# Kernel optimization log

Hardware: AMD Instinct MI355X
Metric: run time of the kernel (lower is better)

Reference implementation:

```python
import jax, jax.numpy as jnp
import numpy as np

B, N, D, H = 2, 384, 128, 8

def _ln(x, g, b, eps=1e-5):
    m = jnp.mean(x, -1, keepdims=True)
    v = jnp.mean((x - m) ** 2, -1, keepdims=True)
    return (x - m) * jax.lax.rsqrt(v + eps) * g + b

def _gelu(x):
    return jax.nn.gelu(x, approximate=False)  # torch nn.GELU default = exact erf

def setup_inputs() -> dict:
    key = jax.random.key(0)
    ks = jax.random.split(key, 20)
    def w(i, *s):
        return jax.random.normal(ks[i], s, jnp.float32) * 0.02
    return {
        'node_features': jax.random.normal(ks[0], (B, N, D), jnp.float32),
        'edge_features': jax.random.normal(ks[1], (B, N, N, D), jnp.float32),
        'mask': jnp.ones((B, N), dtype=bool),
        'attn_wqkv_node': w(2, D, 3 * D),
        'attn_wqkv_edge': w(3, D, 4 * D),
        'lin0_w': w(4, D, D), 'lin0_b': jnp.zeros(D, jnp.float32),
        'ln0_g': jnp.ones(D, jnp.float32), 'ln0_bias': jnp.zeros(D, jnp.float32),
        'ln1_g': jnp.ones(D, jnp.float32), 'ln1_bias': jnp.zeros(D, jnp.float32),
        'nmlp_w1': w(5, D, 2 * D), 'nmlp_w2': w(6, 2 * D, D), 'nmlp_b2': jnp.zeros(D, jnp.float32),
        'e0_we': w(7, 2 * D, D), 'e0_be': jnp.zeros(D, jnp.float32),
        'e0_ws': w(8, D, D), 'e0_bs': jnp.zeros(D, jnp.float32),
        'e0_wt': w(9, D, D), 'e0_bt': jnp.zeros(D, jnp.float32),
        'e0_wer': w(10, D, D), 'e0_wec': w(11, D, D),
        'e0_w1': w(12, D, D), 'e0_b1': jnp.zeros(D, jnp.float32),
        'e1_w1': w(13, D, 2 * D), 'e1_w2': w(14, 2 * D, D), 'e1_b2': jnp.zeros(D, jnp.float32),
        'eln0_g': jnp.ones(D, jnp.float32), 'eln0_b': jnp.zeros(D, jnp.float32),
        'eln1_g': jnp.ones(D, jnp.float32), 'eln1_b': jnp.zeros(D, jnp.float32),
    }

def _forward(node, edge, wqkv_n, wqkv_e, lin0_w, lin0_b, ln0_g, ln0_bias, ln1_g, ln1_bias,
             nmlp_w1, nmlp_w2, nmlp_b2, e0_we, e0_be, e0_ws, e0_bs, e0_wt, e0_bt,
             e0_wer, e0_wec, e0_w1, e0_b1, e1_w1, e1_w2, e1_b2, eln0_g, eln0_b, eln1_g, eln1_b):
    b, n, d = node.shape
    h = H
    dh = d // h
    scale = 1.0 / (d ** 0.5)  # note: scale uses full d_hid as in source
    # ---- RTAttention (modulate_v=True) ----
    qkv_n = (node @ wqkv_n).reshape(b, n, h, 3 * dh).transpose(0, 2, 1, 3)  # b h n 3dh
    qn, kn, vn = jnp.split(qkv_n, 3, axis=-1)
    qkv_e = (edge @ wqkv_e).reshape(b, n, n, h, 4 * dh).transpose(0, 3, 1, 2, 4)  # b h i j 4dh
    eq, ek, ev, em = jnp.split(qkv_e, 4, axis=-1)
    q = qn[:, :, :, None, :] + eq                      # b h i j dh
    k = kn[:, :, None, :, :] + ek
    v = vn[:, :, None, :, :] * em + ev                 # modulate_v: v_node*edge[3] + edge[2]
    dots = scale * jnp.einsum('bhijd,bhijd->bhij', q, k)
    attn = jax.nn.softmax(dots, axis=-1)
    out = jnp.einsum('bhij,bhijd->bhid', attn, v)
    out = out.transpose(0, 2, 1, 3).reshape(b, n, d)
    # ---- node updates, type 'rt' (dropout=0 -> identity) ----
    x = _ln(node + (out @ lin0_w + lin0_b), ln0_g, ln0_bias)
    x = _ln(x + (_gelu(x @ nmlp_w1) @ nmlp_w2 + nmlp_b2), ln1_g, ln1_bias)
    # ---- edge updates: EdgeMLP ----
    sn = (x @ e0_ws + e0_bs)[:, :, None, :]                       # broadcast over j
    tn = (x @ e0_wt + e0_bt)[:, None, :, :]                       # broadcast over i
    se = jnp.mean(edge, axis=1, keepdims=True) @ e0_wec           # mean over dim -3, lin0_ec
    te = jnp.mean(edge, axis=2, keepdims=True) @ e0_wer           # mean over dim -2, lin0_er
    e = jnp.concatenate([edge, jnp.swapaxes(edge, 1, 2)], axis=-1) @ e0_we + e0_be
    e = _gelu(e + sn + tn + se + te) @ e0_w1 + e0_b1
    edge2 = _ln(edge + e, eln0_g, eln0_b)
    edge2 = _ln(edge2 + (_gelu(edge2 @ e1_w1) @ e1_w2 + e1_b2), eln1_g, eln1_b)
    return x, edge2

def reference(node_features, edge_features, mask, attn_wqkv_node, attn_wqkv_edge,
              lin0_w, lin0_b, ln0_g, ln0_bias, ln1_g, ln1_bias,
              nmlp_w1, nmlp_w2, nmlp_b2, e0_we, e0_be, e0_ws, e0_bs, e0_wt, e0_bt,
              e0_wer, e0_wec, e0_w1, e0_b1, e1_w1, e1_w2, e1_b2,
              eln0_g, eln0_b, eln1_g, eln1_b):
    # mask is accepted but unused by the source forward path
    return _forward(node_features, edge_features, attn_wqkv_node, attn_wqkv_edge,
                    lin0_w, lin0_b, ln0_g, ln0_bias, ln1_g, ln1_bias,
                    nmlp_w1, nmlp_w2, nmlp_b2, e0_we, e0_be, e0_ws, e0_bs, e0_wt, e0_bt,
                    e0_wer, e0_wec, e0_w1, e0_b1, e1_w1, e1_w2, e1_b2,
                    eln0_g, eln0_b, eln1_g, eln1_b)
```

## Files before the change

### kernel.cpp

```cpp
#include <hip/hip_runtime.h>
#include <hip/hip_bf16.h>
#include <cstdint>
#include <cstddef>

#define B_ 2
#define N_ 384
#define D_ 128
#define NN (N_*N_)
#define BN (B_*N_)
#define EDGE_ELEMS (B_*NN*D_)
#define NODE_ELEMS (BN*D_)

typedef short bh8 __attribute__((ext_vector_type(8)));
typedef float f32x4 __attribute__((ext_vector_type(4)));

__device__ __forceinline__ f32x4 mfma_bf16(bh8 a, bh8 b, f32x4 c){
  return __builtin_amdgcn_mfma_f32_16x16x32_bf16(a, b, c, 0, 0, 0);
}
__device__ __forceinline__ unsigned short f2bf(float f){
  unsigned u = __float_as_uint(f);
  return (unsigned short)((u + 0x7fffu + ((u >> 16) & 1u)) >> 16);
}
__device__ __forceinline__ unsigned f2bf_pk(float a, float b){
  __hip_bfloat162 h = __float22bfloat162_rn(make_float2(a, b));
  return *(unsigned*)&h;
}
__device__ __forceinline__ float bf2f(unsigned short h){
  return __uint_as_float(((unsigned)h) << 16);
}
__device__ __forceinline__ float geluf(float x){
  return 0.5f * x * (1.0f + erff(x * 0.70710678118654752f));
}
__device__ __forceinline__ float gelu_fast(float x){
  float x2 = x * x;
  float t  = __fmaf_rn(0.044715f * x, x2, x);
  float e  = __expf(1.5957691216057308f * t);
  float r  = __builtin_amdgcn_rcpf(e + 1.0f);
  return x - x * r;
}
__device__ __forceinline__ f32x4 zero4(){ f32x4 z = {0.f,0.f,0.f,0.f}; return z; }

__global__ void kprep(const float* wqkv_e, const float* e0_we, const float* e0_w1,
                      const float* e1_w1, const float* e1_w2,
                      const float* node, const float* wqkv_n,
                      unsigned short* WqkvT, unsigned short* WeT, unsigned short* W1T,
                      unsigned short* E1W1T, unsigned short* E1W2T,
                      float* qkvn){
  int m = blockIdx.y;
  int tid = threadIdx.x;
  if (m < 5){
    const float* src; unsigned short* dst; int K, Nn;
    if (m == 0){ src = wqkv_e; dst = WqkvT; K = 128; Nn = 512; }
    else if (m == 1){ src = e0_we; dst = WeT;   K = 256; Nn = 128; }
    else if (m == 2){ src = e0_w1; dst = W1T;   K = 128; Nn = 128; }
    else if (m == 3){ src = e1_w1; dst = E1W1T; K = 128; Nn = 256; }
    else            { src = e1_w2; dst = E1W2T; K = 256; Nn = 128; }
    int idx = blockIdx.x * 384 + tid;
    if (idx < K * Nn){
      int n = idx / K, k = idx % K;
      dst[idx] = f2bf(src[k * Nn + n]);
    }
  } else {
    int row = blockIdx.x;
    __shared__ float sn[128];
    if (tid < 128) sn[tid] = node[row * 128 + tid];
    __syncthreads();
    float acc = 0.f;
    #pragma unroll 8
    for (int k = 0; k < 128; ++k) acc += sn[k] * wqkv_n[k * 384 + tid];
    qkvn[row * 384 + tid] = acc;
  }
}

__global__ void kprepA(const float* __restrict__ edge, unsigned short* __restrict__ E16,
                       float* __restrict__ meanJ){
  __shared__ float red[8][128];
  int bi = blockIdx.x; int tid = threadIdx.x;
  const float4* src = (const float4*)(edge + (size_t)bi * N_ * D_);
  uint2* gdst = (uint2*)E16 + (size_t)bi * (N_ * D_ / 4);
  float ps0 = 0.f, ps1 = 0.f, ps2 = 0.f, ps3 = 0.f;
  #pragma unroll 4
  for (int k = 0; k < 48; ++k){
    int idx = k * 256 + tid;
    float4 v = src[idx];
    uint2 o;
    o.x = f2bf_pk(v.x, v.y);
    o.y = f2bf_pk(v.z, v.w);
    gdst[idx] = o;
    ps0 += v.x; ps1 += v.y; ps2 += v.z; ps3 += v.w;
  }
  int g = tid >> 5, d0 = (tid & 31) * 4;
  red[g][d0] = ps0; red[g][d0 + 1] = ps1; red[g][d0 + 2] = ps2; red[g][d0 + 3] = ps3;
  __syncthreads();
  if (tid < 128){
    float s = 0.f;
    #pragma unroll
    for (int gg = 0; gg < 8; ++gg) s += red[gg][tid];
    meanJ[bi * 128 + tid] = s * (1.0f / N_);
  }
}

__global__ __launch_bounds__(256, 2) void kattnI(
    const unsigned short* __restrict__ E16, const unsigned short* __restrict__ WqkvT,
    const float* __restrict__ qkvn, float* __restrict__ attn,
    float* __restrict__ meanI){
  __shared__ float red[16][128];
  int tid = threadIdx.x;
  if (blockIdx.y == 1){
    int bj = blockIdx.x; int b = bj / N_, j = bj % N_;
    int ig = tid >> 4, dsub = tid & 15;
    float acc[8];
    #pragma unroll
    for (int e = 0; e < 8; ++e) acc[e] = 0.f;
    #pragma unroll 4
    for (int i = ig; i < N_; i += 16){
      const unsigned short* p = E16 + ((size_t)(b * N_ + i) * N_ + j) * D_ + dsub * 8;
      uint4 u = *(const uint4*)p;
      acc[0] += bf2f((unsigned short)(u.x & 0xffff)); acc[1] += bf2f((unsigned short)(u.x >> 16));
      acc[2] += bf2f((unsigned short)(u.y & 0xffff)); acc[3] += bf2f((unsigned short)(u.y >> 16));
      acc[4] += bf2f((unsigned short)(u.z & 0xffff)); acc[5] += bf2f((unsigned short)(u.z >> 16));
      acc[6] += bf2f((unsigned short)(u.w & 0xffff)); acc[7] += bf2f((unsigned short)(u.w >> 16));
    }
    #pragma unroll
    for (int e = 0; e < 8; ++e) red[ig][dsub * 8 + e] = acc[e];
    __syncthreads();
    if (tid < 128){
      float s = 0.f;
      #pragma unroll
      for (int gg = 0; gg < 16; ++gg) s += red[gg][tid];
      meanI[bj * 128 + tid] = s * (1.0f / N_);
    }
    return;
  }
  int bi = blockIdx.x; int b = bi / N_;
  int w = tid >> 6, lane = tid & 63, quad = lane >> 4, c16 = lane & 15;
  const float scale = 0.08838834764831845f;
  const unsigned short* Abase = E16 + (size_t)bi * N_ * D_;

  bh8 bf[2][4][4];
  #pragma unroll
  for (int s = 0; s < 2; ++s){
    int h = w + s * 4;
    #pragma unroll
    for (int u = 0; u < 4; ++u)
      #pragma unroll
      for (int ks = 0; ks < 4; ++ks){
        int col = h * 64 + u * 16 + c16;
        bf[s][u][ks] = *(const bh8*)(WqkvT + col * 128 + ks * 32 + quad * 8);
      }
  }
  float qv[2];
  #pragma unroll
  for (int s = 0; s < 2; ++s) qv[s] = qkvn[bi * 384 + (w + s * 4) * 48 + c16];

  float m_run[2] = {-1e30f, -1e30f}, l_run[2] = {0.f, 0.f}, o[2] = {0.f, 0.f};
  bh8 af[4];
  #pragma unroll
  for (int ks = 0; ks < 4; ++ks)
    af[ks] = *(const bh8*)(Abase + (size_t)c16 * D_ + ks * 32 + quad * 8);

  for (int jt = 0; jt < 24; ++jt){
    int jn = (jt + 1 < 24) ? jt + 1 : 0;
    bh8 afn[4];
    #pragma unroll
    for (int ks = 0; ks < 4; ++ks)
      afn[ks] = *(const bh8*)(Abase + (size_t)(jn * 16 + c16) * D_ + ks * 32 + quad * 8);
    float knv[2][4], vnv[2][4];
    const float* kvb = qkvn + ((size_t)b * N_ + jt * 16 + quad * 4) * 384;
    #pragma unroll
    for (int s = 0; s < 2; ++s)
      #pragma unroll
      for (int r = 0; r < 4; ++r){
        knv[s][r] = kvb[r * 384 + (w + s * 4) * 48 + 16 + c16];
        vnv[s][r] = kvb[r * 384 + (w + s * 4) * 48 + 32 + c16];
      }
    f32x4 EQ[2], EK[2], EV[2], EM[2];
    #pragma unroll
    for (int s = 0; s < 2; ++s){ EQ[s] = zero4(); EK[s] = zero4(); EV[s] = zero4(); EM[s] = zero4(); }
    #pragma unroll
    for (int ks = 0; ks < 4; ++ks)
      #pragma unroll
      for (int s = 0; s < 2; ++s){
        EQ[s] = mfma_bf16(af[ks], bf[s][0][ks], EQ[s]);
        EK[s] = mfma_bf16(af[ks], bf[s][1][ks], EK[s]);
        EV[s] = mfma_bf16(af[ks], bf[s][2][ks], EV[s]);
        EM[s] = mfma_bf16(af[ks], bf[s][3][ks], EM[s]);
      }
    #pragma unroll
    for (int s = 0; s < 2; ++s){
      float dots[4], vv[4];
      #pragma unroll
      for (int r = 0; r < 4; ++r){
        float t1 = (qv[s] + EQ[s][r]) * (knv[s][r] + EK[s][r]);
        t1 += __shfl_xor(t1, 1); t1 += __shfl_xor(t1, 2);
        t1 += __shfl_xor(t1, 4); t1 += __shfl_xor(t1, 8);
        dots[r] = t1 * scale;
        vv[r] = vnv[s][r] * EM[s][r] + EV[s][r];
      }
      float tmax = fmaxf(fmaxf(dots[0], dots[1]), fmaxf(dots[2], dots[3]));
      tmax = fmaxf(tmax, __shfl_xor(tmax, 16));
      tmax = fmaxf(tmax, __shfl_xor(tmax, 32));
      float mnew = fmaxf(m_run[s], tmax);
      float al = __expf(m_run[s] - mnew);
      float p0 = __expf(dots[0] - mnew), p1 = __expf(dots[1] - mnew);
      float p2 = __expf(dots[2] - mnew), p3 = __expf(dots[3] - mnew);
      float lt = p0 + p1 + p2 + p3;
      lt += __shfl_xor(lt, 16); lt += __shfl_xor(lt, 32);
      l_run[s] = l_run[s] * al + lt;
      m_run[s] = mnew;
      o[s] = o[s] * al + p0 * vv[0] + p1 * vv[1] + p2 * vv[2] + p3 * vv[3];
    }
    #pragma unroll
    for (int ks = 0; ks < 4; ++ks) af[ks] = afn[ks];
  }
  #pragma unroll
  for (int s = 0; s < 2; ++s){
    float oo = o[s];
    oo += __shfl_xor(oo, 16); oo += __shfl_xor(oo, 32);
    oo /= l_run[s];
    if (quad == 0) attn[(size_t)bi * D_ + (w + s * 4) * 16 + c16] = oo;
  }
}

__global__ void knodeadd(const float* __restrict__ node, const float* __restrict__ attn,
                         const float* lin0_w, const float* lin0_b,
                         const float* g0, const float* bb0,
                         const float* w1, const float* w2, const float* b2,
                         const float* g1, const float* bb1,
                         const float* __restrict__ meanJ, const float* __restrict__ meanI,
                         const float* ws, const float* bs, const float* wt, const float* bt,
                         const float* wer, const float* wec, const float* be,
                         float* __restrict__ xOut,
                         float* __restrict__ rowAdd, float* __restrict__ colAdd){
  int row = blockIdx.x; int tid = threadIdx.x;
  __shared__ float sa[128], sx[128], sh[256], rb[8], sx2[128], smJ[128], smI[128];
  if (tid < 128){
    sa[tid] = attn[row * 128 + tid];
    smJ[tid] = meanJ[row * 128 + tid];
    smI[tid] = meanI[row * 128 + tid];
  }
  __syncthreads();
  float y = 0.f, x0 = 0.f;
  if (tid < 128){
    float acc = lin0_b[tid];
    #pragma unroll 8
    for (int k = 0; k < 128; ++k) acc += sa[k] * lin0_w[k * 128 + tid];
    y = acc + node[row * 128 + tid];
  }
  { float sv = (tid < 128) ? y : 0.f, sq = (tid < 128) ? y * y : 0.f;
    #pragma unroll
    for (int m2 = 32; m2 >= 1; m2 >>= 1){ sv += __shfl_xor(sv, m2); sq += __shfl_xor(sq, m2); }
    if ((tid & 63) == 0){ rb[tid >> 6] = sv; rb[4 + (tid >> 6)] = sq; } }
  __syncthreads();
  float mean = (rb[0] + rb[1] + rb[2] + rb[3]) * (1.f / 128.f);
  float var  = (rb[4] + rb[5] + rb[6] + rb[7]) * (1.f / 128.f) - mean * mean;
  float rstd = rsqrtf(var + 1e-5f);
  if (tid < 128){ x0 = (y - mean) * rstd * g0[tid] + bb0[tid]; sx[tid] = x0; }
  __syncthreads();
  { float acc = 0.f;
    #pragma unroll 8
    for (int k = 0; k < 128; ++k) acc += sx[k] * w1[k * 256 + tid];
    sh[tid] = geluf(acc); }
  __syncthreads();
  float y2 = 0.f;
  if (tid < 128){
    float acc = b2[tid];
    #pragma unroll 8
    for (int e = 0; e < 256; ++e) acc += sh[e] * w2[e * 128 + tid];
    y2 = acc + x0;
  }
  __syncthreads();
  { float sv = (tid < 128) ? y2 : 0.f, sq = (tid < 128) ? y2 * y2 : 0.f;
    #pragma unroll
    for (int m2 = 32; m2 >= 1; m2 >>= 1){ sv += __shfl_xor(sv, m2); sq += __shfl_xor(sq, m2); }
    if ((tid & 63) == 0){ rb[tid >> 6] = sv; rb[4 + (tid >> 6)] = sq; } }
  __syncthreads();
  mean = (rb[0] + rb[1] + rb[2] + rb[3]) * (1.f / 128.f);
  var  = (rb[4] + rb[5] + rb[6] + rb[7]) * (1.f / 128.f) - mean * mean;
  rstd = rsqrtf(var + 1e-5f);
  if (tid < 128){
    float xv = (y2 - mean) * rstd * g1[tid] + bb1[tid];
    xOut[row * 128 + tid] = xv;
    sx2[tid] = xv;
  }
  __syncthreads();
  if (tid < 128){
    int d = tid;
    float s1 = bs[d], s3 = 0.f;
    #pragma unroll 8
    for (int k = 0; k < 128; ++k){
      s1 += sx2[k] * ws[k * 128 + d];
      s3 += smJ[k] * wer[k * 128 + d];
    }
    rowAdd[row * 128 + d] = s1 + s3 + be[d];
  } else {
    int d = tid - 128;
    float s2 = bt[d], s4 = 0.f;
    #pragma unroll 8
    for (int k = 0; k < 128; ++k){
      s2 += sx2[k] * wt[k * 128 + d];
      s4 += smI[k] * wec[k * 128 + d];
    }
    colAdd[row * 128 + d] = s2 + s4;
  }
}

__global__ __launch_bounds__(256, 3) void kedge4(
    const unsigned short* __restrict__ E16, const unsigned short* __restrict__ WeT,
    const unsigned short* __restrict__ W1T, const unsigned short* __restrict__ E1W1T,
    const unsigned short* __restrict__ E1W2T,
    const float* __restrict__ rowAdd, const float* __restrict__ colAdd,
    const float* __restrict__ b1, const float* __restrict__ eg0, const float* __restrict__ eb0,
    const float* __restrict__ e1b2, const float* __restrict__ eg1, const float* __restrict__ eb1,
    float* __restrict__ eOut){
  __shared__ unsigned short sA[64][264];
  __shared__ unsigned short sT[64][136];
  __shared__ float lrS[4][64], lrQ[4][64];
  int tid = threadIdx.x;
  int w = tid >> 6, lane = tid & 63, quad = lane >> 4, c16 = lane & 15;
  int R0 = blockIdx.x * 64;
  int b = R0 / NN; int rem = R0 % NN; int i = rem / N_; int j0 = rem % N_;

  bh8 wb1[2][8];
  #pragma unroll
  for (int t = 0; t < 2; ++t)
    #pragma unroll
    for (int ks = 0; ks < 8; ++ks){
      int col = w * 32 + t * 16 + c16;
      wb1[t][ks] = *(const bh8*)(WeT + (size_t)col * 256 + ks * 32 + quad * 8);
    }
  float ca[2][16], rAv[2];
  #pragma unroll
  for (int t = 0; t < 2; ++t){
    rAv[t] = rowAdd[(b * N_ + i) * D_ + w * 32 + t * 16 + c16];
    #pragma unroll
    for (int ms = 0; ms < 4; ++ms)
      #pragma unroll
      for (int r = 0; r < 4; ++r)
        ca[t][ms * 4 + r] = colAdd[(size_t)(b * N_ + j0 + ms * 16 + quad * 4 + r) * D_
                                   + w * 32 + t * 16 + c16];
  }

  #pragma unroll
  for (int it = 0; it < 8; ++it){
    int cid = it * 256 + tid;
    int rrow = cid >> 5;
    int kc = (cid & 31) * 8;
    const unsigned short* sp;
    if (kc < 128) sp = E16 + ((size_t)(b * N_ + i) * N_ + (j0 + rrow)) * D_ + kc;
    else          sp = E16 + ((size_t)(b * N_ + j0 + rrow) * N_ + i) * D_ + (kc - 128);
    *(float4*)&sA[rrow][kc] = *(const float4*)sp;
  }
  __syncthreads();

  f32x4 acc1[2][4];
  #pragma unroll
  for (int t = 0; t < 2; ++t) for (int ms = 0; ms < 4; ++ms) acc1[t][ms] = zero4();
  #pragma unroll
  for (int ks = 0; ks < 8; ++ks){
    bh8 af[4];
    #pragma unroll
    for (int ms = 0; ms < 4; ++ms)
      af[ms] = *(const bh8*)&sA[ms * 16 + c16][ks * 32 + quad * 8];
    #pragma unroll
    for (int t = 0; t < 2; ++t)
      #pragma unroll
      for (int ms = 0; ms < 4; ++ms)
        acc1[t][ms] = mfma_bf16(af[ms], wb1[t][ks], acc1[t][ms]);
  }
  #pragma unroll
  for (int ms = 0; ms < 4; ++ms)
    #pragma unroll
    for (int r = 0; r < 4; ++r){
      int m = ms * 16 + quad * 4 + r;
      float v0 = gelu_fast(acc1[0][ms][r] + rAv[0] + ca[0][ms * 4 + r]);
      float v1 = gelu_fast(acc1[1][ms][r] + rAv[1] + ca[1][ms * 4 + r]);
      unsigned pk = f2bf_pk(v0, v1);
      sT[m][w * 32 + c16] = (unsigned short)(pk & 0xffff);
      sT[m][w * 32 + 16 + c16] = (unsigned short)(pk >> 16);
    }
  __syncthreads();

  bh8 wb2[2][4];
  #pragma unroll
  for (int t = 0; t < 2; ++t)
    #pragma unroll
    for (int ks = 0; ks < 4; ++ks){
      int col = w * 32 + t * 16 + c16;
      wb2[t][ks] = *(const bh8*)(W1T + (size_t)col * 128 + ks * 32 + quad * 8);
    }
  f32x4 acc2[2][4];
  #pragma unroll
  for (int t = 0; t < 2; ++t) for (int ms = 0; ms < 4; ++ms) acc2[t][ms] = zero4();
  #pragma unroll
  for (int ks = 0; ks < 4; ++ks){
    bh8 af[4];
    #pragma unroll
    for (int ms = 0; ms < 4; ++ms)
      af[ms] = *(const bh8*)&sT[ms * 16 + c16][ks * 32 + quad * 8];
    #pragma unroll
    for (int t = 0; t < 2; ++t)
      #pragma unroll
      for (int ms = 0; ms < 4; ++ms)
        acc2[t][ms] = mfma_bf16(af[ms], wb2[t][ks], acc2[t][ms]);
  }
  float b1v[2], g0v[2], b0v[2];
  #pragma unroll
  for (int t = 0; t < 2; ++t){
    int c = w * 32 + t * 16 + c16;
    b1v[t] = b1[c]; g0v[t] = eg0[c]; b0v[t] = eb0[c];
  }
  #pragma unroll
  for (int ms = 0; ms < 4; ++ms)
    #pragma unroll
    for (int r = 0; r < 4; ++r){
      int m = ms * 16 + quad * 4 + r;
      float s = 0.f, q = 0.f;
      #pragma unroll
      for (int t = 0; t < 2; ++t){
        float v = acc2[t][ms][r] + b1v[t] + bf2f(sA[m][w * 32 + t * 16 + c16]);
        acc2[t][ms][r] = v; s += v; q += v * v;
      }
      s += __shfl_xor(s, 1); s += __shfl_xor(s, 2); s += __shfl_xor(s, 4); s += __shfl_xor(s, 8);
      q += __shfl_xor(q, 1); q += __shfl_xor(q, 2); q += __shfl_xor(q, 4); q += __shfl_xor(q, 8);
      if (c16 == 0){ lrS[w][m] = s; lrQ[w][m] = q; }
    }
  __syncthreads();

  #pragma unroll
  for (int ms = 0; ms < 4; ++ms)
    #pragma unroll
    for (int r = 0; r < 4; ++r){
      int m = ms * 16 + quad * 4 + r;
      float s = lrS[0][m] + lrS[1][m] + lrS[2][m] + lrS[3][m];
      float q = lrQ[0][m] + lrQ[1][m] + lrQ[2][m] + lrQ[3][m];
      float mean = s * (1.f / 128.f);
      float var  = q * (1.f / 128.f) - mean * mean;
      float rstd = rsqrtf(var + 1e-5f);
      float e0 = (acc2[0][ms][r] - mean) * rstd * g0v[0] + b0v[0];
      float e1 = (acc2[1][ms][r] - mean) * rstd * g0v[1] + b0v[1];
      unsigned pk = f2bf_pk(e0, e1);
      sA[m][w * 32 + c16] = (unsigned short)(pk & 0xffff);
      sA[m][w * 32 + 16 + c16] = (unsigned short)(pk >> 16);
    }
  __syncthreads();

  f32x4 acc4[2][4];
  #pragma unroll
  for (int t = 0; t < 2; ++t) for (int ms = 0; ms < 4; ++ms) acc4[t][ms] = zero4();
  #pragma unroll
  for (int p = 0; p < 2; ++p){
    bh8 wb3[2][4];
    #pragma unroll
    for (int t = 0; t < 2; ++t)
      #pragma unroll
      for (int ks = 0; ks < 4; ++ks){
        int col = p * 128 + w * 32 + t * 16 + c16;
        wb3[t][ks] = *(const bh8*)(E1W1T + (size_t)col * 128 + ks * 32 + quad * 8);
      }
    f32x4 acc3[2][4];
    #pragma unroll
    for (int t = 0; t < 2; ++t) for (int ms = 0; ms < 4; ++ms) acc3[t][ms] = zero4();
    #pragma unroll
    for (int ks = 0; ks < 4; ++ks){
      bh8 af[4];
      #pragma unroll
      for (int ms = 0; ms < 4; ++ms)
        af[ms] = *(const bh8*)&sA[ms * 16 + c16][ks * 32 + quad * 8];
      #pragma unroll
      for (int t = 0; t < 2; ++t)
        #pragma unroll
        for (int ms = 0; ms < 4; ++ms)
          acc3[t][ms] = mfma_bf16(af[ms], wb3[t][ks], acc3[t][ms]);
    }
    #pragma unroll
    for (int ms = 0; ms < 4; ++ms)
      #pragma unroll
      for (int r = 0; r < 4; ++r){
        int m = ms * 16 + quad * 4 + r;
        float v0 = gelu_fast(acc3[0][ms][r]);
        float v1 = gelu_fast(acc3[1][ms][r]);
        unsigned pk = f2bf_pk(v0, v1);
        sT[m][w * 32 + c16] = (unsigned short)(pk & 0xffff);
        sT[m][w * 32 + 16 + c16] = (unsigned short)(pk >> 16);
      }
    __syncthreads();
    bh8 wb4[2][4];
    #pragma unroll
    for (int t = 0; t < 2; ++t)
      #pragma unroll
      for (int k2 = 0; k2 < 4; ++k2){
        int col = w * 32 + t * 16 + c16;
        wb4[t][k2] = *(const bh8*)(E1W2T + (size_t)col * 256 + p * 128 + k2 * 32 + quad * 8);
      }
    #pragma unroll
    for (int k2 = 0; k2 < 4; ++k2){
      bh8 af[4];
      #pragma unroll
      for (int ms = 0; ms < 4; ++ms)
        af[ms] = *(const bh8*)&sT[ms * 16 + c16][k2 * 32 + quad * 8];
      #pragma unroll
      for (int t = 0; t < 2; ++t)
        #pragma unroll
        for (int ms = 0; ms < 4; ++ms)
          acc4[t][ms] = mfma_bf16(af[ms], wb4[t][k2], acc4[t][ms]);
    }
    __syncthreads();
  }

  float b2v[2], g1v[2], bb1v[2];
  #pragma unroll
  for (int t = 0; t < 2; ++t){
    int c = w * 32 + t * 16 + c16;
    b2v[t] = e1b2[c]; g1v[t] = eg1[c]; bb1v[t] = eb1[c];
  }
  #pragma unroll
  for (int ms = 0; ms < 4; ++ms)
    #pragma unroll
    for (int r = 0; r < 4; ++r){
      int m = ms * 16 + quad * 4 + r;
      float s = 0.f, q = 0.f;
      #pragma unroll
      for (int t = 0; t < 2; ++t){
        float v = acc4[t][ms][r] + b2v[t] + bf2f(sA[m][w * 32 + t * 16 + c16]);
        acc4[t][ms][r] = v; s += v; q += v * v;
      }
      s += __shfl_xor(s, 1); s += __shfl_xor(s, 2); s += __shfl_xor(s, 4); s += __shfl_xor(s, 8);
      q += __shfl_xor(q, 1); q += __shfl_xor(q, 2); q += __shfl_xor(q, 4); q += __shfl_xor(q, 8);
      if (c16 == 0){ lrS[w][m] = s; lrQ[w][m] = q; }
    }
  __syncthreads();
  float* outBase = eOut + ((size_t)(b * N_ + i) * N_ + j0) * D_;
  #pragma unroll
  for (int ms = 0; ms < 4; ++ms)
    #pragma unroll
    for (int r = 0; r < 4; ++r){
      int m = ms * 16 + quad * 4 + r;
      float s = lrS[0][m] + lrS[1][m] + lrS[2][m] + lrS[3][m];
      float q = lrQ[0][m] + lrQ[1][m] + lrQ[2][m] + lrQ[3][m];
      float mean = s * (1.f / 128.f);
      float var  = q * (1.f / 128.f) - mean * mean;
      float rstd = rsqrtf(var + 1e-5f);
      #pragma unroll
      for (int t = 0; t < 2; ++t){
        int c = w * 32 + t * 16 + c16;
        outBase[(size_t)m * D_ + c] = (acc4[t][ms][r] - mean) * rstd * g1v[t] + bb1v[t];
      }
    }
}

extern "C" void kernel_launch(void* const* d_in, const int* in_sizes, int n_in,
                              void* d_out, int out_size, void* d_ws, size_t ws_size,
                              hipStream_t stream){
  const float* node   = (const float*)d_in[0];
  const float* edge   = (const float*)d_in[1];
  const float* wqkv_n = (const float*)d_in[3];
  const float* wqkv_e = (const float*)d_in[4];
  const float* lin0_w = (const float*)d_in[5];
  const float* lin0_b = (const float*)d_in[6];
  const float* ln0_g  = (const float*)d_in[7];
  const float* ln0_b  = (const float*)d_in[8];
  const float* ln1_g  = (const float*)d_in[9];
  const float* ln1_b  = (const float*)d_in[10];
  const float* nmlp_w1= (const float*)d_in[11];
  const float* nmlp_w2= (const float*)d_in[12];
  const float* nmlp_b2= (const float*)d_in[13];
  const float* e0_we  = (const float*)d_in[14];
  const float* e0_be  = (const float*)d_in[15];
  const float* e0_ws  = (const float*)d_in[16];
  const float* e0_bs  = (const float*)d_in[17];
  const float* e0_wt  = (const float*)d_in[18];
  const float* e0_bt  = (const float*)d_in[19];
  const float* e0_wer = (const float*)d_in[20];
  const float* e0_wec = (const float*)d_in[21];
  const float* e0_w1  = (const float*)d_in[22];
  const float* e0_b1  = (const float*)d_in[23];
  const float* e1_w1  = (const float*)d_in[24];
  const float* e1_w2  = (const float*)d_in[25];
  const float* e1_b2  = (const float*)d_in[26];
  const float* eln0_g = (const float*)d_in[27];
  const float* eln0_b = (const float*)d_in[28];
  const float* eln1_g = (const float*)d_in[29];
  const float* eln1_b = (const float*)d_in[30];

  unsigned short* E16   = (unsigned short*)d_ws;
  unsigned short* WqkvT = E16 + (size_t)EDGE_ELEMS;
  unsigned short* WeT   = WqkvT + 65536;
  unsigned short* W1T   = WeT + 32768;
  unsigned short* E1W1T = W1T + 16384;
  unsigned short* E1W2T = E1W1T + 32768;
  float* fbase  = (float*)(E1W2T + 32768);
  float* qkvn   = fbase;
  float* attn   = qkvn + (size_t)BN * 384;
  float* meanJ  = attn + NODE_ELEMS;
  float* meanI  = meanJ + NODE_ELEMS;
  float* rowAdd = meanI + NODE_ELEMS;
  float* colAdd = rowAdd + NODE_ELEMS;

  float* xOut = (float*)d_out;
  float* eOut = xOut + NODE_ELEMS;

  kprep<<<dim3(BN, 6), 384, 0, stream>>>(wqkv_e, e0_we, e0_w1, e1_w1, e1_w2,
                                         node, wqkv_n,
                                         WqkvT, WeT, W1T, E1W1T, E1W2T, qkvn);
  kprepA<<<BN, 256, 0, stream>>>(edge, E16, meanJ);
  kattnI<<<dim3(BN, 2), 256, 0, stream>>>(E16, WqkvT, qkvn, attn, meanI);
  knodeadd<<<BN, 256, 0, stream>>>(node, attn, lin0_w, lin0_b, ln0_g, ln0_b,
                                   nmlp_w1, nmlp_w2, nmlp_b2, ln1_g, ln1_b,
                                   meanJ, meanI, e0_ws, e0_bs, e0_wt, e0_bt,
                                   e0_wer, e0_wec, e0_be,
                                   xOut, rowAdd, colAdd);
  kedge4<<<NN * B_ / 64, 256, 0, stream>>>(E16, WeT, W1T, E1W1T, E1W2T,
                                           rowAdd, colAdd, e0_b1,
                                           eln0_g, eln0_b, e1_b2, eln1_g, eln1_b,
                                           eOut);
}
```

Measured before the change: 640.4 us.

## Split kedge4 columns across 8 waves and alias LayerNorm scratch into sT

The fused edge kernel moves from 4 waves covering 32 output columns each to 8 waves covering 16 columns each (512 threads per block). This halves the per-thread accumulator and weight-fragment registers so more waves can be resident to hide latency. The per-row LayerNorm reduction scratch now lives inside the sT shared buffer, and a two-stage cross-wave reduction writes mean/rstd to a shared stats array. The cost is an extra barrier per LayerNorm, smaller per-wave MFMA batches, and each A fragment being read from LDS by twice as many waves.

Result: slower. 667.0 us (+4.2%).

```diff
diff --git a/kernel.cpp b/kernel.cpp
--- a/kernel.cpp
+++ b/kernel.cpp
@@ -305,7 +305,7 @@
   }
 }
 
-__global__ __launch_bounds__(256, 3) void kedge4(
+__global__ __launch_bounds__(512, 6) void kedge4(
     const unsigned short* __restrict__ E16, const unsigned short* __restrict__ WeT,
     const unsigned short* __restrict__ W1T, const unsigned short* __restrict__ E1W1T,
     const unsigned short* __restrict__ E1W2T,
@@ -315,35 +315,18 @@
     float* __restrict__ eOut){
   __shared__ unsigned short sA[64][264];
   __shared__ unsigned short sT[64][136];
-  __shared__ float lrS[4][64], lrQ[4][64];
+  float*  lrS   = (float*)&sT[0][0];
+  float*  lrQ   = lrS + 8 * 72;
+  float2* stats = (float2*)(lrQ + 8 * 72);
   int tid = threadIdx.x;
   int w = tid >> 6, lane = tid & 63, quad = lane >> 4, c16 = lane & 15;
+  int c = w * 16 + c16;
   int R0 = blockIdx.x * 64;
   int b = R0 / NN; int rem = R0 % NN; int i = rem / N_; int j0 = rem % N_;
 
-  bh8 wb1[2][8];
-  #pragma unroll
-  for (int t = 0; t < 2; ++t)
-    #pragma unroll
-    for (int ks = 0; ks < 8; ++ks){
-      int col = w * 32 + t * 16 + c16;
-      wb1[t][ks] = *(const bh8*)(WeT + (size_t)col * 256 + ks * 32 + quad * 8);
-    }
-  float ca[2][16], rAv[2];
-  #pragma unroll
-  for (int t = 0; t < 2; ++t){
-    rAv[t] = rowAdd[(b * N_ + i) * D_ + w * 32 + t * 16 + c16];
-    #pragma unroll
-    for (int ms = 0; ms < 4; ++ms)
-      #pragma unroll
-      for (int r = 0; r < 4; ++r)
-        ca[t][ms * 4 + r] = colAdd[(size_t)(b * N_ + j0 + ms * 16 + quad * 4 + r) * D_
-                                   + w * 32 + t * 16 + c16];
-  }
-
-  #pragma unroll
-  for (int it = 0; it < 8; ++it){
-    int cid = it * 256 + tid;
+  #pragma unroll
+  for (int it = 0; it < 4; ++it){
+    int cid = it * 512 + tid;
     int rrow = cid >> 5;
     int kc = (cid & 31) * 8;
     const unsigned short* sp;
@@ -351,11 +334,15 @@
     else          sp = E16 + ((size_t)(b * N_ + j0 + rrow) * N_ + i) * D_ + (kc - 128);
     *(float4*)&sA[rrow][kc] = *(const float4*)sp;
   }
-  __syncthreads();
-
-  f32x4 acc1[2][4];
-  #pragma unroll
-  for (int t = 0; t < 2; ++t) for (int ms = 0; ms < 4; ++ms) acc1[t][ms] = zero4();
+  bh8 wb1[8];
+  #pragma unroll
+  for (int ks = 0; ks < 8; ++ks)
+    wb1[ks] = *(const bh8*)(WeT + (size_t)c * 256 + ks * 32 + quad * 8);
+  __syncthreads();
+
+  f32x4 acc1[4];
+  #pragma unroll
+  for (int ms = 0; ms < 4; ++ms) acc1[ms] = zero4();
   #pragma unroll
   for (int ks = 0; ks < 8; ++ks){
     bh8 af[4];
@@ -363,35 +350,33 @@
     for (int ms = 0; ms < 4; ++ms)
       af[ms] = *(const bh8*)&sA[ms * 16 + c16][ks * 32 + quad * 8];
     #pragma unroll
-    for (int t = 0; t < 2; ++t)
-      #pragma unroll
-      for (int ms = 0; ms < 4; ++ms)
-        acc1[t][ms] = mfma_bf16(af[ms], wb1[t][ks], acc1[t][ms]);
-  }
-  #pragma unroll
-  for (int ms = 0; ms < 4; ++ms)
-    #pragma unroll
-    for (int r = 0; r < 4; ++r){
-      int m = ms * 16 + quad * 4 + r;
-      float v0 = gelu_fast(acc1[0][ms][r] + rAv[0] + ca[0][ms * 4 + r]);
-      float v1 = gelu_fast(acc1[1][ms][r] + rAv[1] + ca[1][ms * 4 + r]);
-      unsigned pk = f2bf_pk(v0, v1);
-      sT[m][w * 32 + c16] = (unsigned short)(pk & 0xffff);
-      sT[m][w * 32 + 16 + c16] = (unsigned short)(pk >> 16);
-    }
-  __syncthreads();
-
-  bh8 wb2[2][4];
-  #pragma unroll
-  for (int t = 0; t < 2; ++t)
-    #pragma unroll
-    for (int ks = 0; ks < 4; ++ks){
-      int col = w * 32 + t * 16 + c16;
-      wb2[t][ks] = *(const bh8*)(W1T + (size_t)col * 128 + ks * 32 + quad * 8);
-    }
-  f32x4 acc2[2][4];
-  #pragma unroll
-  for (int t = 0; t < 2; ++t) for (int ms = 0; ms < 4; ++ms) acc2[t][ms] = zero4();
+    for (int ms = 0; ms < 4; ++ms)
+      acc1[ms] = mfma_bf16(af[ms], wb1[ks], acc1[ms]);
+  }
+  float rAv = rowAdd[(b * N_ + i) * D_ + c];
+  float ca[16];
+  #pragma unroll
+  for (int ms = 0; ms < 4; ++ms)
+    #pragma unroll
+    for (int r = 0; r < 4; ++r)
+      ca[ms * 4 + r] = colAdd[(size_t)(b * N_ + j0 + ms * 16 + quad * 4 + r) * D_ + c];
+  #pragma unroll
+  for (int ms = 0; ms < 4; ++ms)
+    #pragma unroll
+    for (int r = 0; r < 4; ++r){
+      int m = ms * 16 + quad * 4 + r;
+      float v = gelu_fast(acc1[ms][r] + rAv + ca[ms * 4 + r]);
+      sT[m][c] = f2bf(v);
+    }
+  __syncthreads();
+
+  bh8 wb2[4];
+  #pragma unroll
+  for (int ks = 0; ks < 4; ++ks)
+    wb2[ks] = *(const bh8*)(W1T + (size_t)c * 128 + ks * 32 + quad * 8);
+  f32x4 acc2[4];
+  #pragma unroll
+  for (int ms = 0; ms < 4; ++ms) acc2[ms] = zero4();
   #pragma unroll
   for (int ks = 0; ks < 4; ++ks){
     bh8 af[4];
@@ -399,68 +384,63 @@
     for (int ms = 0; ms < 4; ++ms)
       af[ms] = *(const bh8*)&sT[ms * 16 + c16][ks * 32 + quad * 8];
     #pragma unroll
-    for (int t = 0; t < 2; ++t)
-      #pragma unroll
-      for (int ms = 0; ms < 4; ++ms)
-        acc2[t][ms] = mfma_bf16(af[ms], wb2[t][ks], acc2[t][ms]);
-  }
-  float b1v[2], g0v[2], b0v[2];
-  #pragma unroll
-  for (int t = 0; t < 2; ++t){
-    int c = w * 32 + t * 16 + c16;
-    b1v[t] = b1[c]; g0v[t] = eg0[c]; b0v[t] = eb0[c];
-  }
-  #pragma unroll
-  for (int ms = 0; ms < 4; ++ms)
-    #pragma unroll
-    for (int r = 0; r < 4; ++r){
-      int m = ms * 16 + quad * 4 + r;
-      float s = 0.f, q = 0.f;
-      #pragma unroll
-      for (int t = 0; t < 2; ++t){
-        float v = acc2[t][ms][r] + b1v[t] + bf2f(sA[m][w * 32 + t * 16 + c16]);
-        acc2[t][ms][r] = v; s += v; q += v * v;
-      }
+    for (int ms = 0; ms < 4; ++ms)
+      acc2[ms] = mfma_bf16(af[ms], wb2[ks], acc2[ms]);
+  }
+  float b1v = b1[c], g0v = eg0[c], b0v = eb0[c];
+  #pragma unroll
+  for (int ms = 0; ms < 4; ++ms)
+    #pragma unroll
+    for (int r = 0; r < 4; ++r){
+      int m = ms * 16 + quad * 4 + r;
+      acc2[ms][r] = acc2[ms][r] + b1v + bf2f(sA[m][c]);
+    }
+  __syncthreads();
+  #pragma unroll
+  for (int ms = 0; ms < 4; ++ms)
+    #pragma unroll
+    for (int r = 0; r < 4; ++r){
+      int m = ms * 16 + quad * 4 + r;
+      float s = acc2[ms][r], q = s * s;
       s += __shfl_xor(s, 1); s += __shfl_xor(s, 2); s += __shfl_xor(s, 4); s += __shfl_xor(s, 8);
       q += __shfl_xor(q, 1); q += __shfl_xor(q, 2); q += __shfl_xor(q, 4); q += __shfl_xor(q, 8);
-      if (c16 == 0){ lrS[w][m] = s; lrQ[w][m] = q; }
-    }
-  __syncthreads();
-
-  #pragma unroll
-  for (int ms = 0; ms < 4; ++ms)
-    #pragma unroll
-    for (int r = 0; r < 4; ++r){
-      int m = ms * 16 + quad * 4 + r;
-      float s = lrS[0][m] + lrS[1][m] + lrS[2][m] + lrS[3][m];
-      float q = lrQ[0][m] + lrQ[1][m] + lrQ[2][m] + lrQ[3][m];
-      float mean = s * (1.f / 128.f);
-      float var  = q * (1.f / 128.f) - mean * mean;
-      float rstd = rsqrtf(var + 1e-5f);
-      float e0 = (acc2[0][ms][r] - mean) * rstd * g0v[0] + b0v[0];
-      float e1 = (acc2[1][ms][r] - mean) * rstd * g0v[1] + b0v[1];
-      unsigned pk = f2bf_pk(e0, e1);
-      sA[m][w * 32 + c16] = (unsigned short)(pk & 0xffff);
-      sA[m][w * 32 + 16 + c16] = (unsigned short)(pk >> 16);
-    }
-  __syncthreads();
-
-  f32x4 acc4[2][4];
-  #pragma unroll
-  for (int t = 0; t < 2; ++t) for (int ms = 0; ms < 4; ++ms) acc4[t][ms] = zero4();
+      if (c16 == 0){ lrS[w * 72 + m] = s; lrQ[w * 72 + m] = q; }
+    }
+  __syncthreads();
+  {
+    int ww = lane & 7, dd = lane >> 3, mrow = w * 8 + dd;
+    float sp = lrS[ww * 72 + mrow], qp = lrQ[ww * 72 + mrow];
+    sp += __shfl_xor(sp, 1); sp += __shfl_xor(sp, 2); sp += __shfl_xor(sp, 4);
+    qp += __shfl_xor(qp, 1); qp += __shfl_xor(qp, 2); qp += __shfl_xor(qp, 4);
+    float mean = sp * (1.f / 128.f);
+    float var  = qp * (1.f / 128.f) - mean * mean;
+    float rstd = rsqrtf(var + 1e-5f);
+    if (ww == 0) stats[mrow] = make_float2(mean, rstd);
+  }
+  __syncthreads();
+  #pragma unroll
+  for (int ms = 0; ms < 4; ++ms)
+    #pragma unroll
+    for (int r = 0; r < 4; ++r){
+      int m = ms * 16 + quad * 4 + r;
+      float2 st = stats[m];
+      float e0 = (acc2[ms][r] - st.x) * st.y * g0v + b0v;
+      sA[m][c] = f2bf(e0);
+    }
+  __syncthreads();
+
+  f32x4 acc4[4];
+  #pragma unroll
+  for (int ms = 0; ms < 4; ++ms) acc4[ms] = zero4();
   #pragma unroll
   for (int p = 0; p < 2; ++p){
-    bh8 wb3[2][4];
-    #pragma unroll
-    for (int t = 0; t < 2; ++t)
-      #pragma unroll
-      for (int ks = 0; ks < 4; ++ks){
-        int col = p * 128 + w * 32 + t * 16 + c16;
-        wb3[t][ks] = *(const bh8*)(E1W1T + (size_t)col * 128 + ks * 32 + quad * 8);
-      }
-    f32x4 acc3[2][4];
-    #pragma unroll
-    for (int t = 0; t < 2; ++t) for (int ms = 0; ms < 4; ++ms) acc3[t][ms] = zero4();
+    bh8 wb3[4];
+    #pragma unroll
+    for (int ks = 0; ks < 4; ++ks)
+      wb3[ks] = *(const bh8*)(E1W1T + (size_t)(p * 128 + c) * 128 + ks * 32 + quad * 8);
+    f32x4 acc3[4];
+    #pragma unroll
+    for (int ms = 0; ms < 4; ++ms) acc3[ms] = zero4();
     #pragma unroll
     for (int ks = 0; ks < 4; ++ks){
       bh8 af[4];
@@ -468,31 +448,21 @@
       for (int ms = 0; ms < 4; ++ms)
         af[ms] = *(const bh8*)&sA[ms * 16 + c16][ks * 32 + quad * 8];
       #pragma unroll
-      for (int t = 0; t < 2; ++t)
-        #pragma unroll
-        for (int ms = 0; ms < 4; ++ms)
-          acc3[t][ms] = mfma_bf16(af[ms], wb3[t][ks], acc3[t][ms]);
+      for (int ms = 0; ms < 4; ++ms)
+        acc3[ms] = mfma_bf16(af[ms], wb3[ks], acc3[ms]);
     }
     #pragma unroll
     for (int ms = 0; ms < 4; ++ms)
       #pragma unroll
       for (int r = 0; r < 4; ++r){
         int m = ms * 16 + quad * 4 + r;
-        float v0 = gelu_fast(acc3[0][ms][r]);
-        float v1 = gelu_fast(acc3[1][ms][r]);
-        unsigned pk = f2bf_pk(v0, v1);
-        sT[m][w * 32 + c16] = (unsigned short)(pk & 0xffff);
-        sT[m][w * 32 + 16 + c16] = (unsigned short)(pk >> 16);
+        sT[m][c] = f2bf(gelu_fast(acc3[ms][r]));
       }
     __syncthreads();
-    bh8 wb4[2][4];
-    #pragma unroll
-    for (int t = 0; t < 2; ++t)
-      #pragma unroll
-      for (int k2 = 0; k2 < 4; ++k2){
-        int col = w * 32 + t * 16 + c16;
-        wb4[t][k2] = *(const bh8*)(E1W2T + (size_t)col * 256 + p * 128 + k2 * 32 + quad * 8);
-      }
+    bh8 wb4[4];
+    #pragma unroll
+    for (int k2 = 0; k2 < 4; ++k2)
+      wb4[k2] = *(const bh8*)(E1W2T + (size_t)c * 256 + p * 128 + k2 * 32 + quad * 8);
     #pragma unroll
     for (int k2 = 0; k2 < 4; ++k2){
       bh8 af[4];
@@ -500,35 +470,41 @@
       for (int ms = 0; ms < 4; ++ms)
         af[ms] = *(const bh8*)&sT[ms * 16 + c16][k2 * 32 + quad * 8];
       #pragma unroll
-      for (int t = 0; t < 2; ++t)
-        #pragma unroll
-        for (int ms = 0; ms < 4; ++ms)
-          acc4[t][ms] = mfma_bf16(af[ms], wb4[t][k2], acc4[t][ms]);
+      for (int ms = 0; ms < 4; ++ms)
+        acc4[ms] = mfma_bf16(af[ms], wb4[k2], acc4[ms]);
     }
     __syncthreads();
   }
 
-  float b2v[2], g1v[2], bb1v[2];
-  #pragma unroll
-  for (int t = 0; t < 2; ++t){
-    int c = w * 32 + t * 16 + c16;
-    b2v[t] = e1b2[c]; g1v[t] = eg1[c]; bb1v[t] = eb1[c];
-  }
-  #pragma unroll
-  for (int ms = 0; ms < 4; ++ms)
-    #pragma unroll
-    for (int r = 0; r < 4; ++r){
-      int m = ms * 16 + quad * 4 + r;
-      float s = 0.f, q = 0.f;
-      #pragma unroll
-      for (int t = 0; t < 2; ++t){
-        float v = acc4[t][ms][r] + b2v[t] + bf2f(sA[m][w * 32 + t * 16 + c16]);
-        acc4[t][ms][r] = v; s += v; q += v * v;
-      }
+  float b2v = e1b2[c], g1v = eg1[c], bb1v = eb1[c];
+  #pragma unroll
+  for (int ms = 0; ms < 4; ++ms)
+    #pragma unroll
+    for (int r = 0; r < 4; ++r){
+      int m = ms * 16 + quad * 4 + r;
+      acc4[ms][r] = acc4[ms][r] + b2v + bf2f(sA[m][c]);
+    }
+  #pragma unroll
+  for (int ms = 0; ms < 4; ++ms)
+    #pragma unroll
+    for (int r = 0; r < 4; ++r){
+      int m = ms * 16 + quad * 4 + r;
+      float s = acc4[ms][r], q = s * s;
       s += __shfl_xor(s, 1); s += __shfl_xor(s, 2); s += __shfl_xor(s, 4); s += __shfl_xor(s, 8);
       q += __shfl_xor(q, 1); q += __shfl_xor(q, 2); q += __shfl_xor(q, 4); q += __shfl_xor(q, 8);
-      if (c16 == 0){ lrS[w][m] = s; lrQ[w][m] = q; }
-    }
+      if (c16 == 0){ lrS[w * 72 + m] = s; lrQ[w * 72 + m] = q; }
+    }
+  __syncthreads();
+  {
+    int ww = lane & 7, dd = lane >> 3, mrow = w * 8 + dd;
+    float sp = lrS[ww * 72 + mrow], qp = lrQ[ww * 72 + mrow];
+    sp += __shfl_xor(sp, 1); sp += __shfl_xor(sp, 2); sp += __shfl_xor(sp, 4);
+    qp += __shfl_xor(qp, 1); qp += __shfl_xor(qp, 2); qp += __shfl_xor(qp, 4);
+    float mean = sp * (1.f / 128.f);
+    float var  = qp * (1.f / 128.f) - mean * mean;
+    float rstd = rsqrtf(var + 1e-5f);
+    if (ww == 0) stats[mrow] = make_float2(mean, rstd);
+  }
   __syncthreads();
   float* outBase = eOut + ((size_t)(b * N_ + i) * N_ + j0) * D_;
   #pragma unroll
@@ -536,16 +512,8 @@
     #pragma unroll
     for (int r = 0; r < 4; ++r){
       int m = ms * 16 + quad * 4 + r;
-      float s = lrS[0][m] + lrS[1][m] + lrS[2][m] + lrS[3][m];
-      float q = lrQ[0][m] + lrQ[1][m] + lrQ[2][m] + lrQ[3][m];
-      float mean = s * (1.f / 128.f);
-      float var  = q * (1.f / 128.f) - mean * mean;
-      float rstd = rsqrtf(var + 1e-5f);
-      #pragma unroll
-      for (int t = 0; t < 2; ++t){
-        int c = w * 32 + t * 16 + c16;
-        outBase[(size_t)m * D_ + c] = (acc4[t][ms][r] - mean) * rstd * g1v[t] + bb1v[t];
-      }
+      float2 st = stats[m];
+      outBase[(size_t)m * D_ + c] = (acc4[ms][r] - st.x) * st.y * g1v + bb1v;
     }
 }
 
@@ -610,7 +578,7 @@
                                    meanJ, meanI, e0_ws, e0_bs, e0_wt, e0_bt,
                                    e0_wer, e0_wec, e0_be,
                                    xOut, rowAdd, colAdd);
-  kedge4<<<NN * B_ / 64, 256, 0, stream>>>(E16, WeT, W1T, E1W1T, E1W2T,
+  kedge4<<<NN * B_ / 64, 512, 0, stream>>>(E16, WeT, W1T, E1W1T, E1W2T,
                                            rowAdd, colAdd, e0_b1,
                                            eln0_g, eln0_b, e1_b2, eln1_g, eln1_b,
                                            eOut);
```

## Swizzle edge-kernel LDS tiles, use DPP reductions, and share layernorm row stats

Applied to the files above, without the earlier changes.

Replaces the padded shared-memory tiles sA/sT in the edge kernel with unpadded tiles that use an XOR swizzle on 8-element chunks, which avoids LDS bank conflicts and shrinks shared memory per block. Replaces the shuffle-based 16-lane sum reductions with DPP row operations in the attention, node and edge kernels. The per-row layernorm mean and rstd are now computed once per row into a shared stats array, instead of every lane re-summing four partials. This adds an extra barrier, and the swizzle indexing has to stay consistent across every read and write site.

Result: no change. 636.0 us (-0.7%).

```diff
diff --git a/kernel.cpp b/kernel.cpp
--- a/kernel.cpp
+++ b/kernel.cpp
@@ -39,6 +39,22 @@
   return x - x * r;
 }
 __device__ __forceinline__ f32x4 zero4(){ f32x4 z = {0.f,0.f,0.f,0.f}; return z; }
+
+__device__ __forceinline__ float red16_add(float x){
+  x += __int_as_float(__builtin_amdgcn_update_dpp(0, __float_as_int(x), 0xB1, 0xF, 0xF, true));
+  x += __int_as_float(__builtin_amdgcn_update_dpp(0, __float_as_int(x), 0x4E, 0xF, 0xF, true));
+  x += __int_as_float(__builtin_amdgcn_update_dpp(0, __float_as_int(x), 0x141, 0xF, 0xF, true));
+  x += __int_as_float(__builtin_amdgcn_update_dpp(0, __float_as_int(x), 0x140, 0xF, 0xF, true));
+  return x;
+}
+__device__ __forceinline__ float red4_add(float x){
+  x += __int_as_float(__builtin_amdgcn_update_dpp(0, __float_as_int(x), 0xB1, 0xF, 0xF, true));
+  x += __int_as_float(__builtin_amdgcn_update_dpp(0, __float_as_int(x), 0x4E, 0xF, 0xF, true));
+  return x;
+}
+__device__ __forceinline__ int swz(int m, int c){
+  return ((((c >> 3) ^ (m & 7)) << 3) | (c & 7));
+}
 
 __global__ void kprep(const float* wqkv_e, const float* e0_we, const float* e0_w1,
                       const float* e1_w1, const float* e1_w2,
@@ -192,9 +208,7 @@
       #pragma unroll
       for (int r = 0; r < 4; ++r){
         float t1 = (qv[s] + EQ[s][r]) * (knv[s][r] + EK[s][r]);
-        t1 += __shfl_xor(t1, 1); t1 += __shfl_xor(t1, 2);
-        t1 += __shfl_xor(t1, 4); t1 += __shfl_xor(t1, 8);
-        dots[r] = t1 * scale;
+        dots[r] = red16_add(t1) * scale;
         vv[r] = vnv[s][r] * EM[s][r] + EV[s][r];
       }
       float tmax = fmaxf(fmaxf(dots[0], dots[1]), fmaxf(dots[2], dots[3]));
@@ -248,8 +262,9 @@
     y = acc + node[row * 128 + tid];
   }
   { float sv = (tid < 128) ? y : 0.f, sq = (tid < 128) ? y * y : 0.f;
-    #pragma unroll
-    for (int m2 = 32; m2 >= 1; m2 >>= 1){ sv += __shfl_xor(sv, m2); sq += __shfl_xor(sq, m2); }
+    sv = red16_add(sv); sq = red16_add(sq);
+    sv += __shfl_xor(sv, 16); sq += __shfl_xor(sq, 16);
+    sv += __shfl_xor(sv, 32); sq += __shfl_xor(sq, 32);
     if ((tid & 63) == 0){ rb[tid >> 6] = sv; rb[4 + (tid >> 6)] = sq; } }
   __syncthreads();
   float mean = (rb[0] + rb[1] + rb[2] + rb[3]) * (1.f / 128.f);
@@ -271,8 +286,9 @@
   }
   __syncthreads();
   { float sv = (tid < 128) ? y2 : 0.f, sq = (tid < 128) ? y2 * y2 : 0.f;
-    #pragma unroll
-    for (int m2 = 32; m2 >= 1; m2 >>= 1){ sv += __shfl_xor(sv, m2); sq += __shfl_xor(sq, m2); }
+    sv = red16_add(sv); sq = red16_add(sq);
+    sv += __shfl_xor(sv, 16); sq += __shfl_xor(sq, 16);
+    sv += __shfl_xor(sv, 32); sq += __shfl_xor(sq, 32);
     if ((tid & 63) == 0){ rb[tid >> 6] = sv; rb[4 + (tid >> 6)] = sq; } }
   __syncthreads();
   mean = (rb[0] + rb[1] + rb[2] + rb[3]) * (1.f / 128.f);
@@ -313,9 +329,10 @@
     const float* __restrict__ b1, const float* __restrict__ eg0, const float* __restrict__ eb0,
     const float* __restrict__ e1b2, const float* __restrict__ eg1, const float* __restrict__ eb1,
     float* __restrict__ eOut){
-  __shared__ unsigned short sA[64][264];
-  __shared__ unsigned short sT[64][136];
+  __shared__ unsigned short sA[64][256];
+  __shared__ unsigned short sT[64][128];
   __shared__ float lrS[4][64], lrQ[4][64];
+  __shared__ float2 stats[64];
   int tid = threadIdx.x;
   int w = tid >> 6, lane = tid & 63, quad = lane >> 4, c16 = lane & 15;
   int R0 = blockIdx.x * 64;
@@ -345,11 +362,12 @@
   for (int it = 0; it < 8; ++it){
     int cid = it * 256 + tid;
     int rrow = cid >> 5;
-    int kc = (cid & 31) * 8;
+    int chunk = cid & 31;
+    int kc = chunk * 8;
     const unsigned short* sp;
     if (kc < 128) sp = E16 + ((size_t)(b * N_ + i) * N_ + (j0 + rrow)) * D_ + kc;
     else          sp = E16 + ((size_t)(b * N_ + j0 + rrow) * N_ + i) * D_ + (kc - 128);
-    *(float4*)&sA[rrow][kc] = *(const float4*)sp;
+    *(float4*)&sA[rrow][(chunk ^ (rrow & 7)) << 3] = *(const float4*)sp;
   }
   __syncthreads();
 
@@ -361,7 +379,7 @@
     bh8 af[4];
     #pragma unroll
     for (int ms = 0; ms < 4; ++ms)
-      af[ms] = *(const bh8*)&sA[ms * 16 + c16][ks * 32 + quad * 8];
+      af[ms] = *(const bh8*)&sA[ms * 16 + c16][((ks * 4 + quad) ^ (c16 & 7)) << 3];
     #pragma unroll
     for (int t = 0; t < 2; ++t)
       #pragma unroll
@@ -376,8 +394,8 @@
       float v0 = gelu_fast(acc1[0][ms][r] + rAv[0] + ca[0][ms * 4 + r]);
       float v1 = gelu_fast(acc1[1][ms][r] + rAv[1] + ca[1][ms * 4 + r]);
       unsigned pk = f2bf_pk(v0, v1);
-      sT[m][w * 32 + c16] = (unsigned short)(pk & 0xffff);
-      sT[m][w * 32 + 16 + c16] = (unsigned short)(pk >> 16);
+      sT[m][swz(m, w * 32 + c16)]      = (unsigned short)(pk & 0xffff);
+      sT[m][swz(m, w * 32 + 16 + c16)] = (unsigned short)(pk >> 16);
     }
   __syncthreads();
 
@@ -397,7 +415,7 @@
     bh8 af[4];
     #pragma unroll
     for (int ms = 0; ms < 4; ++ms)
-      af[ms] = *(const bh8*)&sT[ms * 16 + c16][ks * 32 + quad * 8];
+      af[ms] = *(const bh8*)&sT[ms * 16 + c16][((ks * 4 + quad) ^ (c16 & 7)) << 3];
     #pragma unroll
     for (int t = 0; t < 2; ++t)
       #pragma unroll
@@ -418,30 +436,35 @@
       float s = 0.f, q = 0.f;
       #pragma unroll
       for (int t = 0; t < 2; ++t){
-        float v = acc2[t][ms][r] + b1v[t] + bf2f(sA[m][w * 32 + t * 16 + c16]);
+        float v = acc2[t][ms][r] + b1v[t] + bf2f(sA[m][swz(m, w * 32 + t * 16 + c16)]);
         acc2[t][ms][r] = v; s += v; q += v * v;
       }
-      s += __shfl_xor(s, 1); s += __shfl_xor(s, 2); s += __shfl_xor(s, 4); s += __shfl_xor(s, 8);
-      q += __shfl_xor(q, 1); q += __shfl_xor(q, 2); q += __shfl_xor(q, 4); q += __shfl_xor(q, 8);
+      s = red16_add(s); q = red16_add(q);
       if (c16 == 0){ lrS[w][m] = s; lrQ[w][m] = q; }
     }
   __syncthreads();
-
+  {
+    int src = lane & 3, mrow = w * 16 + (lane >> 2);
+    float sp = lrS[src][mrow], qp = lrQ[src][mrow];
+    sp = red4_add(sp); qp = red4_add(qp);
+    if (src == 0){
+      float mean = sp * (1.f / 128.f);
+      float var  = qp * (1.f / 128.f) - mean * mean;
+      stats[mrow] = make_float2(mean, rsqrtf(var + 1e-5f));
+    }
+  }
+  __syncthreads();
   #pragma unroll
   for (int ms = 0; ms < 4; ++ms)
     #pragma unroll
     for (int r = 0; r < 4; ++r){
       int m = ms * 16 + quad * 4 + r;
-      float s = lrS[0][m] + lrS[1][m] + lrS[2][m] + lrS[3][m];
-      float q = lrQ[0][m] + lrQ[1][m] + lrQ[2][m] + lrQ[3][m];
-      float mean = s * (1.f / 128.f);
-      float var  = q * (1.f / 128.f) - mean * mean;
-      float rstd = rsqrtf(var + 1e-5f);
-      float e0 = (acc2[0][ms][r] - mean) * rstd * g0v[0] + b0v[0];
-      float e1 = (acc2[1][ms][r] - mean) * rstd * g0v[1] + b0v[1];
+      float2 st = stats[m];
+      float e0 = (acc2[0][ms][r] - st.x) * st.y * g0v[0] + b0v[0];
+      float e1 = (acc2[1][ms][r] - st.x) * st.y * g0v[1] + b0v[1];
       unsigned pk = f2bf_pk(e0, e1);
-      sA[m][w * 32 + c16] = (unsigned short)(pk & 0xffff);
-      sA[m][w * 32 + 16 + c16] = (unsigned short)(pk >> 16);
+      sA[m][swz(m, w * 32 + c16)]      = (unsigned short)(pk & 0xffff);
+      sA[m][swz(m, w * 32 + 16 + c16)] = (unsigned short)(pk >> 16);
     }
   __syncthreads();
 
@@ -466,7 +489,7 @@
       bh8 af[4];
       #pragma unroll
       for (int ms = 0; ms < 4; ++ms)
-        af[ms] = *(const bh8*)&sA[ms * 16 + c16][ks * 32 + quad * 8];
+        af[ms] = *(const bh8*)&sA[ms * 16 + c16][((ks * 4 + quad) ^ (c16 & 7)) << 3];
       #pragma unroll
       for (int t = 0; t < 2; ++t)
         #pragma unroll
@@ -481,8 +504,8 @@
         float v0 = gelu_fast(acc3[0][ms][r]);
         float v1 = gelu_fast(acc3[1][ms][r]);
         unsigned pk = f2bf_pk(v0, v1);
-        sT[m][w * 32 + c16] = (unsigned short)(pk & 0xffff);
-        sT[m][w * 32 + 16 + c16] = (unsigned short)(pk >> 16);
+        sT[m][swz(m, w * 32 + c16)]      = (unsigned short)(pk & 0xffff);
+        sT[m][swz(m, w * 32 + 16 + c16)] = (unsigned short)(pk >> 16);
       }
     __syncthreads();
     bh8 wb4[2][4];
@@ -498,7 +521,7 @@
       bh8 af[4];
       #pragma unroll
       for (int ms = 0; ms < 4; ++ms)
-        af[ms] = *(const bh8*)&sT[ms * 16 + c16][k2 * 32 + quad * 8];
+        af[ms] = *(const bh8*)&sT[ms * 16 + c16][((k2 * 4 + quad) ^ (c16 & 7)) << 3];
       #pragma unroll
       for (int t = 0; t < 2; ++t)
         #pragma unroll
@@ -522,13 +545,23 @@
       float s = 0.f, q = 0.f;
       #pragma unroll
       for (int t = 0; t < 2; ++t){
-        float v = acc4[t][ms][r] + b2v[t] + bf2f(sA[m][w * 32 + t * 16 + c16]);
+        float v = acc4[t][ms][r] + b2v[t] + bf2f(sA[m][swz(m, w * 32 + t * 16 + c16)]);
         acc4[t][ms][r] = v; s += v; q += v * v;
       }
-      s += __shfl_xor(s, 1); s += __shfl_xor(s, 2); s += __shfl_xor(s, 4); s += __shfl_xor(s, 8);
-      q += __shfl_xor(q, 1); q += __shfl_xor(q, 2); q += __shfl_xor(q, 4); q += __shfl_xor(q, 8);
+      s = red16_add(s); q = red16_add(q);
       if (c16 == 0){ lrS[w][m] = s; lrQ[w][m] = q; }
     }
+  __syncthreads();
+  {
+    int src = lane & 3, mrow = w * 16 + (lane >> 2);
+    float sp = lrS[src][mrow], qp = lrQ[src][mrow];
+    sp = red4_add(sp); qp = red4_add(qp);
+    if (src == 0){
+      float mean = sp * (1.f / 128.f);
+      float var  = qp * (1.f / 128.f) - mean * mean;
+      stats[mrow] = make_float2(mean, rsqrtf(var + 1e-5f));
+    }
+  }
   __syncthreads();
   float* outBase = eOut + ((size_t)(b * N_ + i) * N_ + j0) * D_;
   #pragma unroll
@@ -536,15 +569,11 @@
     #pragma unroll
     for (int r = 0; r < 4; ++r){
       int m = ms * 16 + quad * 4 + r;
-      float s = lrS[0][m] + lrS[1][m] + lrS[2][m] + lrS[3][m];
-      float q = lrQ[0][m] + lrQ[1][m] + lrQ[2][m] + lrQ[3][m];
-      float mean = s * (1.f / 128.f);
-      float var  = q * (1.f / 128.f) - mean * mean;
-      float rstd = rsqrtf(var + 1e-5f);
+      float2 st = stats[m];
       #pragma unroll
       for (int t = 0; t < 2; ++t){
         int c = w * 32 + t * 16 + c16;
-        outBase[(size_t)m * D_ + c] = (acc4[t][ms][r] - mean) * rstd * g1v[t] + bb1v[t];
+        outBase[(size_t)m * D_ + c] = (acc4[t][ms][r] - st.x) * st.y * g1v[t] + bb1v[t];
       }
     }
 }
```
